# Optimization experiments

Measured on AMD Instinct MI355X. Metric: run time of the kernel, lower is better.

## Reference

```python
import jax, jax.numpy as jnp
import numpy as np

N = 50000       # nodes
E = 800000      # edges (avg degree 16)
D_IN = 128      # input_dim
H = 256         # hidden_dim
Z = H // 2      # 128, latent / conv3-4 width
D_OUT = 64      # output_dim


def _glorot(key, shape):
    fan_in, fan_out = shape
    lim = float(np.sqrt(6.0 / (fan_in + fan_out)))
    return jax.random.uniform(key, shape, jnp.float32, -lim, lim)


def setup_inputs() -> dict:
    key = jax.random.key(0)
    ks = jax.random.split(key, 16)
    inp = {
        "x": jax.random.uniform(ks[0], (N, D_IN), jnp.float32),
        "edge_index": jax.random.randint(ks[1], (2, E), 0, N, jnp.int32),
        "epsilon": jax.random.normal(ks[2], (N, Z), jnp.float32),
        # SAGEConv params: Wl (neighbor/aggr path, with bias), Wr (root path, no bias)
        "Wl1": _glorot(ks[3], (D_IN, H)), "bl1": jnp.zeros((H,), jnp.float32), "Wr1": _glorot(ks[4], (D_IN, H)),
        "Wl2": _glorot(ks[5], (H, H)),    "bl2": jnp.zeros((H,), jnp.float32), "Wr2": _glorot(ks[6], (H, H)),
        "Wl3": _glorot(ks[7], (Z, Z)),    "bl3": jnp.zeros((Z,), jnp.float32), "Wr3": _glorot(ks[8], (Z, Z)),
        "Wl4": _glorot(ks[9], (Z, Z)),    "bl4": jnp.zeros((Z,), jnp.float32), "Wr4": _glorot(ks[10], (Z, Z)),
        "W_lin": _glorot(ks[11], (Z, D_OUT)), "b_lin": jnp.zeros((D_OUT,), jnp.float32),
    }
    return inp


def _sage_conv(x, src, dst, Wl, bl, Wr):
    # PyG SAGEConv (mean aggr): out = lin_l(mean_{j in N(i)} x_j) + lin_r(x_i)
    msg = x[src]                                             # [E, d] gather
    agg = jax.ops.segment_sum(msg, dst, num_segments=N)      # [N, d]
    cnt = jax.ops.segment_sum(jnp.ones((src.shape[0],), x.dtype), dst, num_segments=N)
    mean = agg / jnp.maximum(cnt, 1.0)[:, None]
    return mean @ Wl + bl + x @ Wr


def reference(x, edge_index, epsilon,
              Wl1, bl1, Wr1, Wl2, bl2, Wr2,
              Wl3, bl3, Wr3, Wl4, bl4, Wr4,
              W_lin, b_lin):
    src, dst = edge_index[0], edge_index[1]
    h = x / 1000.0 - 0.5
    h = jnp.sin(_sage_conv(h, src, dst, Wl1, bl1, Wr1))      # [N, H]
    h = _sage_conv(h, src, dst, Wl2, bl2, Wr2)               # [N, H]
    mean = h[:, :Z]
    log_var = h[:, Z:]
    z = mean + jnp.exp(log_var) * epsilon                    # reparameterize
    h = jax.nn.relu(_sage_conv(z, src, dst, Wl3, bl3, Wr3))
    h = jax.nn.relu(_sage_conv(h, src, dst, Wl4, bl4, Wr4))
    out = jax.nn.sigmoid(h @ W_lin + b_lin) * 1000.0
    return out, mean, log_var
```

## Files before the change

kernel.cpp:

```cpp
#include <hip/hip_runtime.h>
#include <hip/hip_bf16.h>

#define N_NODES 50000
#define E_EDGES 800000

using u16 = unsigned short;
typedef short bf8 __attribute__((ext_vector_type(8)));
typedef float f32x4 __attribute__((ext_vector_type(4)));

__device__ __forceinline__ float bf2f(u16 h) {
    union { unsigned u; float f; } v;
    v.u = ((unsigned)h) << 16;
    return v.f;
}
__device__ __forceinline__ u16 f2bf(float f) {
    union { float f; unsigned u; } v;
    v.f = f;
    unsigned r = v.u + 0x7FFF + ((v.u >> 16) & 1);
    return (u16)(r >> 16);
}

struct WtArgs {
    const float* src[9];
    u16* dst[9];
    int K[9];
    int N[9];
};

__global__ __launch_bounds__(256) void k_wt(WtArgs a) {
    int wi = blockIdx.y;
    int K = a.K[wi], Nn = a.N[wi];
    int tot = K * Nn;
    for (int i = blockIdx.x * 256 + threadIdx.x; i < tot; i += gridDim.x * 256) {
        int n = i / K, k = i % K;
        a.dst[wi][i] = f2bf(a.src[wi][(size_t)k * Nn + n]);
    }
}

__global__ __launch_bounds__(256) void k_prep(const float* __restrict__ x,
                                              u16* __restrict__ h0) {
    int total = N_NODES * 128 / 4;
    for (int i = blockIdx.x * 256 + threadIdx.x; i < total;
         i += gridDim.x * 256) {
        float4 v = *(const float4*)(x + (size_t)i * 4);
        ushort4 o;
        o.x = f2bf(v.x * 0.001f - 0.5f);
        o.y = f2bf(v.y * 0.001f - 0.5f);
        o.z = f2bf(v.z * 0.001f - 0.5f);
        o.w = f2bf(v.w * 0.001f - 0.5f);
        *(ushort4*)(h0 + (size_t)i * 4) = o;
    }
}

__global__ void k_count(const int* __restrict__ dst, int* __restrict__ deg) {
    for (int i = blockIdx.x * blockDim.x + threadIdx.x; i < E_EDGES;
         i += gridDim.x * blockDim.x)
        atomicAdd(&deg[dst[i]], 1);
}

#define SCAN_B 49

__global__ __launch_bounds__(1024) void k_scan1(const int* __restrict__ deg,
                                                int* __restrict__ bsum) {
    __shared__ int sm[1024];
    int i = blockIdx.x * 1024 + threadIdx.x;
    sm[threadIdx.x] = (i < N_NODES) ? deg[i] : 0;
    __syncthreads();
    for (int ofs = 512; ofs > 0; ofs >>= 1) {
        if (threadIdx.x < ofs) sm[threadIdx.x] += sm[threadIdx.x + ofs];
        __syncthreads();
    }
    if (threadIdx.x == 0) bsum[blockIdx.x] = sm[0];
}

__global__ void k_scan2(const int* __restrict__ bsum, int* __restrict__ bofs) {
    int l = threadIdx.x;
    int v = (l < SCAN_B) ? bsum[l] : 0;
    int orig = v;
    for (int d = 1; d < 64; d <<= 1) {
        int u = __shfl_up(v, d, 64);
        if (l >= d) v += u;
    }
    if (l < SCAN_B) bofs[l] = v - orig;
}

__global__ __launch_bounds__(1024) void k_scan3(const int* __restrict__ deg,
                                                const int* __restrict__ bofs,
                                                int* __restrict__ rowptr,
                                                float* __restrict__ dinv) {
    __shared__ int sm[1024];
    int i = blockIdx.x * 1024 + threadIdx.x;
    int d = (i < N_NODES) ? deg[i] : 0;
    sm[threadIdx.x] = d;
    __syncthreads();
    for (int ofs = 1; ofs < 1024; ofs <<= 1) {
        int u = (threadIdx.x >= (unsigned)ofs) ? sm[threadIdx.x - ofs] : 0;
        __syncthreads();
        sm[threadIdx.x] += u;
        __syncthreads();
    }
    if (i < N_NODES) {
        int incl = sm[threadIdx.x] + bofs[blockIdx.x];
        rowptr[i] = incl - d;
        dinv[i] = 1.0f / fmaxf((float)d, 1.0f);
        if (i == N_NODES - 1) rowptr[N_NODES] = incl;
    }
}

__global__ void k_fill(const int* __restrict__ src, const int* __restrict__ dst,
                       const int* __restrict__ rowptr, int* __restrict__ cursor,
                       int* __restrict__ colidx) {
    for (int i = blockIdx.x * blockDim.x + threadIdx.x; i < E_EDGES;
         i += gridDim.x * blockDim.x) {
        int d = dst[i];
        int pos = rowptr[d] + atomicAdd(&cursor[d], 1);
        colidx[pos] = src[i];
    }
}

template <int D>
__global__ __launch_bounds__(256) void k_aggregate(
    const u16* __restrict__ h, const int* __restrict__ rowptr,
    const int* __restrict__ colidx, const float* __restrict__ dinv,
    u16* __restrict__ mean) {
    constexpr int VA = D / 16;
    int node = (int)((blockIdx.x * 256 + threadIdx.x) >> 6);
    int lane = threadIdx.x & 63;
    if (node >= N_NODES) return;
    int sub = lane >> 4, lr = lane & 15;
    int beg = rowptr[node], end = rowptr[node + 1];
    float acc[VA] = {};
    for (int e = beg + sub; e < end; e += 4) {
        int s = colidx[e];
        const u16* row = h + (size_t)s * D + lr * VA;
        bf8 r0 = *(const bf8*)row;
#pragma unroll
        for (int j = 0; j < 8; ++j) acc[j] += bf2f((u16)r0[j]);
        if (VA == 16) {
            bf8 r1 = *(const bf8*)(row + 8);
#pragma unroll
            for (int j = 0; j < 8; ++j) acc[8 + j] += bf2f((u16)r1[j]);
        }
    }
#pragma unroll
    for (int j = 0; j < VA; ++j) {
        acc[j] += __shfl_xor(acc[j], 16);
        acc[j] += __shfl_xor(acc[j], 32);
    }
    if (sub == 0) {
        float inv = dinv[node];
        u16 outv[VA];
#pragma unroll
        for (int j = 0; j < VA; ++j) outv[j] = f2bf(acc[j] * inv);
        u16* o = mean + (size_t)node * D + lr * VA;
        *(bf8*)o = *(bf8*)&outv[0];
        if (VA == 16) *(bf8*)(o + 8) = *(bf8*)&outv[8];
    }
}

enum { ACT_NONE = 0, ACT_SIN = 1, ACT_RELU = 2, ACT_SIGMOID1000 = 3, ACT_VAE = 4 };

template <int K, int NCB, int NC, int ACT, bool OUT_F32, bool TWO_PASS>
__global__ __launch_bounds__(512) void k_gemm(
    const u16* __restrict__ A1, const u16* __restrict__ Wt1,
    const u16* __restrict__ A2, const u16* __restrict__ Wt2,
    const float* __restrict__ bias, void* __restrict__ Cout,
    float* __restrict__ out_mean, float* __restrict__ out_lv,
    const float* __restrict__ eps) {
    constexpr int PK = K + 8;
    constexpr int M = N_NODES;
    constexpr int CH = K / 8;
    constexpr int NG = NCB / 16;
    extern __shared__ char smem[];
    u16* Bs = (u16*)smem;

    const int t = threadIdx.x;
    const int lane = t & 63;
    const int wave = t >> 6;
    const int lr = lane & 15;
    const int sub = lane >> 4;
    const int y = blockIdx.y;
    const int row0 = (blockIdx.x * 8 + wave) * 16;
    const int arow = row0 + lr;
    const bool rowOK = arow < M;

    auto mapRow = [&](int r) {
        if (ACT == ACT_VAE)
            return r < NCB / 2 ? y * (NCB / 2) + r
                               : NC / 2 + y * (NCB / 2) + (r - NCB / 2);
        return y * NCB + r;
    };

    f32x4 acc[NG];
#pragma unroll
    for (int i = 0; i < NG; ++i) acc[i] = (f32x4){0.f, 0.f, 0.f, 0.f};

    auto pass = [&](const u16* __restrict__ A, const u16* __restrict__ Wt) {
#pragma unroll
        for (int i = 0; i < NCB * CH / 512; ++i) {
            int c = t + i * 512;
            int r = c / CH, kc = c % CH;
            *(bf8*)&Bs[r * PK + kc * 8] =
                *(const bf8*)(Wt + (size_t)mapRow(r) * K + kc * 8);
        }
        const u16* ap = A + (size_t)arow * K + sub * 8;
        bf8 a0 = {0, 0, 0, 0, 0, 0, 0, 0};
        if (rowOK) a0 = *(const bf8*)ap;
        __syncthreads();
#pragma unroll
        for (int ks = 0; ks < K / 32; ++ks) {
            bf8 a = a0;
            if (ks > 0) {
                a = (bf8){0, 0, 0, 0, 0, 0, 0, 0};
                if (rowOK) a = *(const bf8*)(ap + ks * 32);
            }
#pragma unroll
            for (int ni = 0; ni < NG; ++ni) {
                bf8 b = *(const bf8*)&Bs[(ni * 16 + lr) * PK + ks * 32 + sub * 8];
                acc[ni] =
                    __builtin_amdgcn_mfma_f32_16x16x32_bf16(a, b, acc[ni], 0, 0, 0);
            }
        }
        __syncthreads();
    };

    pass(A1, Wt1);
    if (TWO_PASS) pass(A2, Wt2);

    if (ACT == ACT_VAE) {
#pragma unroll
        for (int ni = 0; ni < NG / 2; ++ni) {
            int colm = y * (NCB / 2) + ni * 16 + lr;
            float bm = bias[colm];
            float bl = bias[colm + 128];
#pragma unroll
            for (int r = 0; r < 4; ++r) {
                int row = row0 + sub * 4 + r;
                if (row >= M) continue;
                float mv = acc[ni][r] + bm;
                float lv = acc[ni + NG / 2][r] + bl;
                size_t o = (size_t)row * 128 + colm;
                out_mean[o] = mv;
                out_lv[o] = lv;
                ((u16*)Cout)[o] = f2bf(mv + __expf(lv) * eps[o]);
            }
        }
    } else {
#pragma unroll
        for (int ni = 0; ni < NG; ++ni) {
            int col = y * NCB + ni * 16 + lr;
            float bv = bias[col];
#pragma unroll
            for (int r = 0; r < 4; ++r) {
                int row = row0 + sub * 4 + r;
                if (row >= M) continue;
                float v = acc[ni][r] + bv;
                if (ACT == ACT_SIN) v = __sinf(v);
                else if (ACT == ACT_RELU) v = fmaxf(v, 0.f);
                else if (ACT == ACT_SIGMOID1000) v = 1000.f / (1.f + __expf(-v));
                if (OUT_F32)
                    ((float*)Cout)[(size_t)row * NC + col] = v;
                else
                    ((u16*)Cout)[(size_t)row * NC + col] = f2bf(v);
            }
        }
    }
}

extern "C" void kernel_launch(void* const* d_in, const int* in_sizes, int n_in,
                              void* d_out, int out_size, void* d_ws,
                              size_t ws_size, hipStream_t stream) {
    const int N = N_NODES;
    const float* x = (const float*)d_in[0];
    const int* ei = (const int*)d_in[1];
    const float* eps = (const float*)d_in[2];
    const float* Wl1 = (const float*)d_in[3];
    const float* bl1 = (const float*)d_in[4];
    const float* Wr1 = (const float*)d_in[5];
    const float* Wl2 = (const float*)d_in[6];
    const float* bl2 = (const float*)d_in[7];
    const float* Wr2 = (const float*)d_in[8];
    const float* Wl3 = (const float*)d_in[9];
    const float* bl3 = (const float*)d_in[10];
    const float* Wr3 = (const float*)d_in[11];
    const float* Wl4 = (const float*)d_in[12];
    const float* bl4 = (const float*)d_in[13];
    const float* Wr4 = (const float*)d_in[14];
    const float* W_lin = (const float*)d_in[15];
    const float* b_lin = (const float*)d_in[16];

    const int* src = ei;
    const int* dst = ei + E_EDGES;

    char* w = (char*)d_ws;
    auto alloc = [&](size_t b) {
        void* p = (void*)w;
        w += (b + 255) & ~(size_t)255;
        return p;
    };
    int* deg = (int*)alloc((size_t)N * 4);
    int* rowptr = (int*)alloc((size_t)(N + 1) * 4);
    int* cursor = (int*)alloc((size_t)N * 4);
    int* colidx = (int*)alloc((size_t)E_EDGES * 4);
    float* dinv = (float*)alloc((size_t)N * 4);
    int* bsum = (int*)alloc(64 * 4);
    int* bofs = (int*)alloc(64 * 4);
    u16* hbA = (u16*)alloc((size_t)N * 256 * 2);
    u16* hbB = (u16*)alloc((size_t)N * 256 * 2);
    u16* hbC = (u16*)alloc((size_t)N * 256 * 2);
    static const int wK[9] = {128, 128, 256, 256, 128, 128, 128, 128, 128};
    static const int wN[9] = {256, 256, 256, 256, 128, 128, 128, 128, 64};
    u16* Wt[9];
    for (int i = 0; i < 9; ++i) Wt[i] = (u16*)alloc((size_t)wK[i] * wN[i] * 2);

    float* out_final = (float*)d_out;
    float* out_mean = out_final + (size_t)N * 64;
    float* out_lv = out_mean + (size_t)N * 128;

    hipMemsetAsync(deg, 0, (size_t)N * 4, stream);
    hipMemsetAsync(cursor, 0, (size_t)N * 4, stream);

    WtArgs wa;
    const float* wsrc[9] = {Wl1, Wr1, Wl2, Wr2, Wl3, Wr3, Wl4, Wr4, W_lin};
    for (int i = 0; i < 9; ++i) {
        wa.src[i] = wsrc[i];
        wa.dst[i] = Wt[i];
        wa.K[i] = wK[i];
        wa.N[i] = wN[i];
    }
    k_wt<<<dim3(64, 9), 256, 0, stream>>>(wa);

    k_prep<<<2048, 256, 0, stream>>>(x, hbA);
    k_count<<<3125, 256, 0, stream>>>(dst, deg);
    k_scan1<<<SCAN_B, 1024, 0, stream>>>(deg, bsum);
    k_scan2<<<1, 64, 0, stream>>>(bsum, bofs);
    k_scan3<<<SCAN_B, 1024, 0, stream>>>(deg, bofs, rowptr, dinv);
    k_fill<<<3125, 256, 0, stream>>>(src, dst, rowptr, cursor, colidx);

    const int aggBlocks = (N * 64 + 255) / 256;
    const int gx = (N / 16 + 7) / 8;
    auto shm = [](int NCB, int K) { return (size_t)NCB * (K + 8) * 2; };

    k_aggregate<128><<<aggBlocks, 256, 0, stream>>>(hbA, rowptr, colidx, dinv,
                                                    hbB);
    k_gemm<128, 128, 256, ACT_SIN, false, true>
        <<<dim3(gx, 2), 512, shm(128, 128), stream>>>(hbB, Wt[0], hbA, Wt[1],
                                                      bl1, hbC, nullptr,
                                                      nullptr, nullptr);

    k_aggregate<256><<<aggBlocks, 256, 0, stream>>>(hbC, rowptr, colidx, dinv,
                                                    hbB);
    k_gemm<256, 128, 256, ACT_VAE, false, true>
        <<<dim3(gx, 2), 512, shm(128, 256), stream>>>(hbB, Wt[2], hbC, Wt[3],
                                                      bl2, hbA, out_mean,
                                                      out_lv, eps);

    k_aggregate<128><<<aggBlocks, 256, 0, stream>>>(hbA, rowptr, colidx, dinv,
                                                    hbB);
    k_gemm<128, 64, 128, ACT_RELU, false, true>
        <<<dim3(gx, 2), 512, shm(64, 128), stream>>>(hbB, Wt[4], hbA, Wt[5],
                                                     bl3, hbC, nullptr, nullptr,
                                                     nullptr);

    k_aggregate<128><<<aggBlocks, 256, 0, stream>>>(hbC, rowptr, colidx, dinv,
                                                    hbB);
    k_gemm<128, 64, 128, ACT_RELU, false, true>
        <<<dim3(gx, 2), 512, shm(64, 128), stream>>>(hbB, Wt[6], hbC, Wt[7],
                                                     bl4, hbA, nullptr, nullptr,
                                                     nullptr);

    k_gemm<128, 32, 64, ACT_SIGMOID1000, true, false>
        <<<dim3(gx, 2), 512, shm(32, 128), stream>>>(hbA, Wt[8], nullptr,
                                                     nullptr, b_lin, out_final,
                                                     nullptr, nullptr, nullptr);
}
```

Measured before the change: 380.6 us.

## Unroll aggregate gather by two, prefetch GEMM A fragments, remap blocks per XCD

The aggregation loop now processes two neighbor edges per iteration so that more independent row loads are in flight. The GEMM kernel loads all A fragments for both passes into registers before staging the weights, so global latency overlaps with the LDS staging. It also launches a 1D grid and swizzles block IDs so that the two column halves of a row tile, and neighbouring row tiles, land on the same XCD and can share L2. The costs are higher register pressure from holding the full A fragments and the XCD-count assumption baked into the remap.

Result: no change. 381.1 us (+0.1%).

```diff
diff --git a/kernel.cpp b/kernel.cpp
--- a/kernel.cpp
+++ b/kernel.cpp
@@ -130,7 +130,29 @@
     int sub = lane >> 4, lr = lane & 15;
     int beg = rowptr[node], end = rowptr[node + 1];
     float acc[VA] = {};
-    for (int e = beg + sub; e < end; e += 4) {
+    int e = beg + sub;
+    for (; e + 4 < end; e += 8) {
+        int s0 = colidx[e];
+        int s1 = colidx[e + 4];
+        const u16* p0 = h + (size_t)s0 * D + lr * VA;
+        const u16* p1 = h + (size_t)s1 * D + lr * VA;
+        bf8 r0 = *(const bf8*)p0;
+        bf8 r1 = *(const bf8*)p1;
+        if (VA == 16) {
+            bf8 r0b = *(const bf8*)(p0 + 8);
+            bf8 r1b = *(const bf8*)(p1 + 8);
+#pragma unroll
+            for (int j = 0; j < 8; ++j) {
+                acc[j] += bf2f((u16)r0[j]) + bf2f((u16)r1[j]);
+                acc[8 + j] += bf2f((u16)r0b[j]) + bf2f((u16)r1b[j]);
+            }
+        } else {
+#pragma unroll
+            for (int j = 0; j < 8; ++j)
+                acc[j] += bf2f((u16)r0[j]) + bf2f((u16)r1[j]);
+        }
+    }
+    for (; e < end; e += 4) {
         int s = colidx[e];
         const u16* row = h + (size_t)s * D + lr * VA;
         bf8 r0 = *(const bf8*)row;
@@ -171,16 +193,25 @@
     constexpr int M = N_NODES;
     constexpr int CH = K / 8;
     constexpr int NG = NCB / 16;
+    constexpr int KS = K / 32;
+    constexpr int GX = (M / 16 + 7) / 8;
+    constexpr int NWG = ((GX + 1) / 2) * 2 * 2;
+    constexpr int CPX = NWG / 8;
     extern __shared__ char smem[];
     u16* Bs = (u16*)smem;
+
+    const int bid = blockIdx.x;
+    const int wid = (bid & 7) * CPX + (bid >> 3);
+    const int x = wid >> 1;
+    const int y = wid & 1;
+    if (x >= GX) return;
 
     const int t = threadIdx.x;
     const int lane = t & 63;
     const int wave = t >> 6;
     const int lr = lane & 15;
     const int sub = lane >> 4;
-    const int y = blockIdx.y;
-    const int row0 = (blockIdx.x * 8 + wave) * 16;
+    const int row0 = (x * 8 + wave) * 16;
     const int arow = row0 + lr;
     const bool rowOK = arow < M;
 
@@ -191,11 +222,31 @@
         return y * NCB + r;
     };
 
+    bf8 aF1[KS], aF2[TWO_PASS ? KS : 1];
+    {
+        const u16* ap = A1 + (size_t)arow * K + sub * 8;
+#pragma unroll
+        for (int ks = 0; ks < KS; ++ks) {
+            bf8 a = {0, 0, 0, 0, 0, 0, 0, 0};
+            if (rowOK) a = *(const bf8*)(ap + ks * 32);
+            aF1[ks] = a;
+        }
+    }
+    if (TWO_PASS) {
+        const u16* ap = A2 + (size_t)arow * K + sub * 8;
+#pragma unroll
+        for (int ks = 0; ks < KS; ++ks) {
+            bf8 a = {0, 0, 0, 0, 0, 0, 0, 0};
+            if (rowOK) a = *(const bf8*)(ap + ks * 32);
+            aF2[ks] = a;
+        }
+    }
+
     f32x4 acc[NG];
 #pragma unroll
     for (int i = 0; i < NG; ++i) acc[i] = (f32x4){0.f, 0.f, 0.f, 0.f};
 
-    auto pass = [&](const u16* __restrict__ A, const u16* __restrict__ Wt) {
+    auto stageW = [&](const u16* __restrict__ Wt) {
 #pragma unroll
         for (int i = 0; i < NCB * CH / 512; ++i) {
             int c = t + i * 512;
@@ -203,29 +254,29 @@
             *(bf8*)&Bs[r * PK + kc * 8] =
                 *(const bf8*)(Wt + (size_t)mapRow(r) * K + kc * 8);
         }
-        const u16* ap = A + (size_t)arow * K + sub * 8;
-        bf8 a0 = {0, 0, 0, 0, 0, 0, 0, 0};
-        if (rowOK) a0 = *(const bf8*)ap;
-        __syncthreads();
-#pragma unroll
-        for (int ks = 0; ks < K / 32; ++ks) {
-            bf8 a = a0;
-            if (ks > 0) {
-                a = (bf8){0, 0, 0, 0, 0, 0, 0, 0};
-                if (rowOK) a = *(const bf8*)(ap + ks * 32);
-            }
+    };
+    auto mm = [&](const bf8* aF) {
+#pragma unroll
+        for (int ks = 0; ks < KS; ++ks) {
 #pragma unroll
             for (int ni = 0; ni < NG; ++ni) {
                 bf8 b = *(const bf8*)&Bs[(ni * 16 + lr) * PK + ks * 32 + sub * 8];
                 acc[ni] =
-                    __builtin_amdgcn_mfma_f32_16x16x32_bf16(a, b, acc[ni], 0, 0, 0);
+                    __builtin_amdgcn_mfma_f32_16x16x32_bf16(aF[ks], b, acc[ni],
+                                                            0, 0, 0);
             }
         }
+    };
+
+    stageW(Wt1);
+    __syncthreads();
+    mm(aF1);
+    if (TWO_PASS) {
         __syncthreads();
-    };
-
-    pass(A1, Wt1);
-    if (TWO_PASS) pass(A2, Wt2);
+        stageW(Wt2);
+        __syncthreads();
+        mm(aF2);
+    }
 
     if (ACT == ACT_VAE) {
 #pragma unroll
@@ -338,39 +389,35 @@
     k_fill<<<3125, 256, 0, stream>>>(src, dst, rowptr, cursor, colidx);
 
     const int aggBlocks = (N * 64 + 255) / 256;
-    const int gx = (N / 16 + 7) / 8;
+    const int nwg = 784;
     auto shm = [](int NCB, int K) { return (size_t)NCB * (K + 8) * 2; };
 
     k_aggregate<128><<<aggBlocks, 256, 0, stream>>>(hbA, rowptr, colidx, dinv,
                                                     hbB);
     k_gemm<128, 128, 256, ACT_SIN, false, true>
-        <<<dim3(gx, 2), 512, shm(128, 128), stream>>>(hbB, Wt[0], hbA, Wt[1],
-                                                      bl1, hbC, nullptr,
-                                                      nullptr, nullptr);
+        <<<nwg, 512, shm(128, 128), stream>>>(hbB, Wt[0], hbA, Wt[1], bl1, hbC,
+                                              nullptr, nullptr, nullptr);
 
     k_aggregate<256><<<aggBlocks, 256, 0, stream>>>(hbC, rowptr, colidx, dinv,
                                                     hbB);
     k_gemm<256, 128, 256, ACT_VAE, false, true>
-        <<<dim3(gx, 2), 512, shm(128, 256), stream>>>(hbB, Wt[2], hbC, Wt[3],
-                                                      bl2, hbA, out_mean,
-                                                      out_lv, eps);
+        <<<nwg, 512, shm(128, 256), stream>>>(hbB, Wt[2], hbC, Wt[3], bl2, hbA,
+                                              out_mean, out_lv, eps);
 
     k_aggregate<128><<<aggBlocks, 256, 0, stream>>>(hbA, rowptr, colidx, dinv,
                                                     hbB);
     k_gemm<128, 64, 128, ACT_RELU, false, true>
-        <<<dim3(gx, 2), 512, shm(64, 128), stream>>>(hbB, Wt[4], hbA, Wt[5],
-                                                     bl3, hbC, nullptr, nullptr,
-                                                     nullptr);
+        <<<nwg, 512, shm(64, 128), stream>>>(hbB, Wt[4], hbA, Wt[5], bl3, hbC,
+                                             nullptr, nullptr, nullptr);
 
     k_aggregate<128><<<aggBlocks, 256, 0, stream>>>(hbC, rowptr, colidx, dinv,
                                                     hbB);
     k_gemm<128, 64, 128, ACT_RELU, false, true>
-        <<<dim3(gx, 2), 512, shm(64, 128), stream>>>(hbB, Wt[6], hbC, Wt[7],
-                                                     bl4, hbA, nullptr, nullptr,
-                                                     nullptr);
+        <<<nwg, 512, shm(64, 128), stream>>>(hbB, Wt[6], hbC, Wt[7], bl4, hbA,
+                                             nullptr, nullptr, nullptr);
 
     k_gemm<128, 32, 64, ACT_SIGMOID1000, true, false>
-        <<<dim3(gx, 2), 512, shm(32, 128), stream>>>(hbA, Wt[8], nullptr,
-                                                     nullptr, b_lin, out_final,
-                                                     nullptr, nullptr, nullptr);
-}
+        <<<nwg, 512, shm(32, 128), stream>>>(hbA, Wt[8], nullptr, nullptr,
+                                             b_lin, out_final, nullptr, nullptr,
+                                             nullptr);
+}
```
